# Kernel tuning notes

Measured on AMD Instinct MI355X. Metric: run time of the kernel, lower is better.

## Reference

```python
import jax, jax.numpy as jnp
import numpy as np


def setup_inputs() -> dict:
    key = jax.random.key(0)
    ks = jax.random.split(key, 6)
    B, N, S, D, A = 32, 12, 512, 256, 96
    return {
        "value": jax.random.normal(ks[0], (B, N, S, D), dtype=jnp.float32),
        "emb": jax.random.normal(ks[1], (N, S, A), dtype=jnp.float32),
        "Wqk": jax.random.normal(ks[2], (A, D), dtype=jnp.float32) * (A ** -0.5),
        "bqk": jax.random.normal(ks[3], (D,), dtype=jnp.float32) * 0.02,
        "Wv": jax.random.normal(ks[4], (D, D), dtype=jnp.float32) * (D ** -0.5),
        "bv": jax.random.normal(ks[5], (D,), dtype=jnp.float32) * 0.02,
    }


def reference(value, emb, Wqk, bqk, Wv, bv):
    # qk: [n, s, d] -- query and key share the same projection FC_Q_K
    qk = emb @ Wqk + bqk
    v = value @ Wv + bv                      # [b, n, s, d]
    q = jax.nn.softmax(qk, axis=-1)          # softmax over d (last dim of query)
    k = jax.nn.softmax(qk.swapaxes(-1, -2), axis=-1)  # [n, d, s], softmax over s
    # key @ value: [n, d, s] x [b, n, s, e] -> [b, n, d, e] (broadcast over b)
    kv = jnp.einsum('nds,bnse->bnde', k, v)
    # query @ kv: [n, s, d] x [b, n, d, e] -> [b, n, s, e]
    out = jnp.einsum('nsd,bnde->bnse', q, kv)
    return out
```

## Files before the change

kernel.cpp:

```cpp
#include <hip/hip_runtime.h>
#include <hip/hip_bf16.h>

#define B_ 32
#define N_ 12
#define S_ 512
#define D_ 256
#define A_ 96

typedef __attribute__((ext_vector_type(8))) short short8;
typedef __attribute__((ext_vector_type(4))) float float4v;

static __device__ __forceinline__ ushort f2bf(float f) {
  union { float f; unsigned u; } a;
  a.f = f;
  return (ushort)((a.u + 0x7FFFu + ((a.u >> 16) & 1u)) >> 16);
}

__global__ __launch_bounds__(256) void k_qk_softmax_q(
    const float* __restrict__ emb, const float* __restrict__ Wqk,
    const float* __restrict__ bqk, float* __restrict__ qk,
    ushort* __restrict__ qb) {
  const int blk = blockIdx.x;
  const int tid = threadIdx.x;
  const int d = tid;
  const int wv = tid >> 6, lane = tid & 63;
  __shared__ float seT[A_][8];
  __shared__ float redm[8][4], reds[8][4];
  const float* ebase = emb + (size_t)blk * 8 * A_;
  for (int k = tid; k < 8 * A_; k += 256) {
    int r = k / A_, a = k - r * A_;
    seT[a][r] = ebase[k];
  }
  __syncthreads();
  float bq = bqk[d];
  float acc[8];
#pragma unroll
  for (int r = 0; r < 8; ++r) acc[r] = bq;
#pragma unroll 8
  for (int a = 0; a < A_; ++a) {
    float w = Wqk[a * D_ + d];
    float4 lo = *(const float4*)(&seT[a][0]);
    float4 hi = *(const float4*)(&seT[a][4]);
    acc[0] = fmaf(lo.x, w, acc[0]);
    acc[1] = fmaf(lo.y, w, acc[1]);
    acc[2] = fmaf(lo.z, w, acc[2]);
    acc[3] = fmaf(lo.w, w, acc[3]);
    acc[4] = fmaf(hi.x, w, acc[4]);
    acc[5] = fmaf(hi.y, w, acc[5]);
    acc[6] = fmaf(hi.z, w, acc[6]);
    acc[7] = fmaf(hi.w, w, acc[7]);
  }
  const size_t obase = (size_t)blk * 8 * D_ + d;
#pragma unroll
  for (int r = 0; r < 8; ++r) qk[obase + r * D_] = acc[r];
  float m[8];
#pragma unroll
  for (int r = 0; r < 8; ++r) {
    m[r] = acc[r];
    for (int off = 32; off; off >>= 1) m[r] = fmaxf(m[r], __shfl_xor(m[r], off));
  }
  if (lane == 0) {
#pragma unroll
    for (int r = 0; r < 8; ++r) redm[r][wv] = m[r];
  }
  __syncthreads();
  float e[8], s[8];
#pragma unroll
  for (int r = 0; r < 8; ++r) {
    float mm = fmaxf(fmaxf(redm[r][0], redm[r][1]),
                     fmaxf(redm[r][2], redm[r][3]));
    e[r] = __expf(acc[r] - mm);
    s[r] = e[r];
    for (int off = 32; off; off >>= 1) s[r] += __shfl_xor(s[r], off);
  }
  if (lane == 0) {
#pragma unroll
    for (int r = 0; r < 8; ++r) reds[r][wv] = s[r];
  }
  __syncthreads();
#pragma unroll
  for (int r = 0; r < 8; ++r) {
    float sum = reds[r][0] + reds[r][1] + reds[r][2] + reds[r][3];
    qb[obase + r * D_] = f2bf(e[r] / sum);
  }
}

__global__ __launch_bounds__(256) void k_softmax_kT(
    const float* __restrict__ qk, ushort* __restrict__ kTb) {
  const int dc = blockIdx.x * 16;
  const int n = blockIdx.y;
  const int tid = threadIdx.x;
  __shared__ float t[16][514];
  const float* base = qk + (size_t)n * S_ * D_ + dc;
#pragma unroll
  for (int it = 0; it < 8; ++it) {
    int id = it * 256 + tid;
    int d4 = id & 3, s = id >> 2;
    float4 v = *(const float4*)(base + (size_t)s * D_ + 4 * d4);
    t[4 * d4 + 0][s] = v.x;
    t[4 * d4 + 1][s] = v.y;
    t[4 * d4 + 2][s] = v.z;
    t[4 * d4 + 3][s] = v.w;
  }
  __syncthreads();
  const int d = tid >> 4, sg = tid & 15;
  float vv[32];
  float m = -1e30f;
#pragma unroll
  for (int k = 0; k < 32; ++k) {
    vv[k] = t[d][sg + 16 * k];
    m = fmaxf(m, vv[k]);
  }
  for (int off = 1; off < 16; off <<= 1) m = fmaxf(m, __shfl_xor(m, off));
  float sum = 0.0f;
#pragma unroll
  for (int k = 0; k < 32; ++k) {
    vv[k] = __expf(vv[k] - m);
    sum += vv[k];
  }
  for (int off = 1; off < 16; off <<= 1) sum += __shfl_xor(sum, off);
  float inv = 1.0f / sum;
  const size_t ob = ((size_t)n * D_ + dc + d) * S_;
#pragma unroll
  for (int k = 0; k < 32; ++k) kTb[ob + sg + 16 * k] = f2bf(vv[k] * inv);
}

__global__ __launch_bounds__(256) void k_wvt(const float* __restrict__ Wv,
                                             ushort* __restrict__ WvT) {
  int c = blockIdx.x, e = threadIdx.x;
  WvT[c * D_ + e] = f2bf(Wv[e * D_ + c]);
}

__global__ __launch_bounds__(512) void k_kv0(
    const ushort* __restrict__ kTb, const float* __restrict__ value,
    ushort* __restrict__ kv0) {
  const int f = blockIdx.x;
  const int wk = (f & 7) * 192 + (f >> 3);
  const int eq = wk & 3;
  const int bz = wk >> 2;
  const int n = bz % N_;
  const int tid = threadIdx.x;
  const int l = tid & 63, w = tid >> 6;
  const int lane16 = l & 15, quad = l >> 4;

  __shared__ ushort ldsV[2][64 * 72];

  const int se = tid & 63;
  const int sch = tid >> 6;
  const int schs = (sch ^ ((se >> 3) & 7)) << 3;
  const float* vbase = value + (size_t)bz * S_ * D_ + eq * 64 + se;
  const ushort* kTbase = kTb + (size_t)n * D_ * S_ + (w * 32) * S_;

  float4v acc[4][2];
#pragma unroll
  for (int i = 0; i < 4; ++i)
#pragma unroll
    for (int j = 0; j < 2; ++j) acc[i][j] = (float4v)0.0f;

  union Pack { ushort u[8]; uint4 v; };

  {
    float f0[8];
#pragma unroll
    for (int t = 0; t < 8; ++t) f0[t] = vbase[(size_t)(sch * 8 + t) * D_];
    Pack pk;
#pragma unroll
    for (int t = 0; t < 8; ++t) pk.u[t] = f2bf(f0[t]);
    *(uint4*)(&ldsV[0][se * 72 + schs]) = pk.v;
  }

  int p = 0;
  for (int sc = 0; sc < S_; sc += 64) {
    __syncthreads();
    float fs[8];
    const bool more = (sc + 64 < S_);
    if (more) {
#pragma unroll
      for (int t = 0; t < 8; ++t)
        fs[t] = vbase[(size_t)(sc + 64 + sch * 8 + t) * D_];
    }
#pragma unroll
    for (int kc = 0; kc < 64; kc += 32) {
      const int ko = kc + quad * 8;
      const int chr = ko >> 3;
      short8 a[4], b[2];
#pragma unroll
      for (int i = 0; i < 4; ++i) {
        int er = i * 16 + lane16;
        a[i] = *(const short8*)(
            &ldsV[p][er * 72 + ((chr ^ ((er >> 3) & 7)) << 3)]);
      }
#pragma unroll
      for (int j = 0; j < 2; ++j)
        b[j] = *(const short8*)(kTbase + (j * 16 + lane16) * S_ + sc + ko);
#pragma unroll
      for (int i = 0; i < 4; ++i)
#pragma unroll
        for (int j = 0; j < 2; ++j)
          acc[i][j] = __builtin_amdgcn_mfma_f32_16x16x32_bf16(a[i], b[j],
                                                              acc[i][j], 0, 0, 0);
    }
    if (more) {
      Pack pk;
#pragma unroll
      for (int t = 0; t < 8; ++t) pk.u[t] = f2bf(fs[t]);
      *(uint4*)(&ldsV[p ^ 1][se * 72 + schs]) = pk.v;
    }
    p ^= 1;
  }
  ushort* obase = kv0 + (size_t)bz * D_ * D_;
#pragma unroll
  for (int i = 0; i < 4; ++i) {
#pragma unroll
    for (int j = 0; j < 2; ++j) {
      int d = w * 32 + j * 16 + lane16;
      int e0 = eq * 64 + i * 16 + quad * 4;
      ushort4 pk;
      pk.x = f2bf(acc[i][j][0]);
      pk.y = f2bf(acc[i][j][1]);
      pk.z = f2bf(acc[i][j][2]);
      pk.w = f2bf(acc[i][j][3]);
      *(ushort4*)(obase + d * D_ + e0) = pk;
    }
  }
}

__global__ __launch_bounds__(256) void k_kvw_inplace(
    ushort* kv0, const ushort* __restrict__ WvT,
    const float* __restrict__ bv) {
  const int qd = blockIdx.x;
  const int bz = blockIdx.y;
  const int tid = threadIdx.x;
  const int l = tid & 63, w = tid >> 6;
  const int lane16 = l & 15, quad = l >> 4;

  __shared__ ushort ldsA[64 * 72];
  __shared__ ushort ldsB[256 * 72];

  float4v acc[4][4];
#pragma unroll
  for (int i = 0; i < 4; ++i)
#pragma unroll
    for (int j = 0; j < 4; ++j) acc[i][j] = (float4v)0.0f;

  ushort* base = kv0 + (size_t)bz * (D_ * D_) + qd * (64 * D_);

  for (int ec = 0; ec < D_; ec += 64) {
    __syncthreads();
#pragma unroll
    for (int it = 0; it < 2; ++it) {
      int id = it * 256 + tid;
      int rd = id >> 3, cc = (id & 7) * 8;
      *(uint4*)(&ldsA[rd * 72 + cc]) =
          *(const uint4*)(base + rd * D_ + ec + cc);
    }
#pragma unroll
    for (int it = 0; it < 8; ++it) {
      int id = it * 256 + tid;
      int rd = id >> 3, cc = (id & 7) * 8;
      *(uint4*)(&ldsB[rd * 72 + cc]) =
          *(const uint4*)(WvT + rd * D_ + ec + cc);
    }
    __syncthreads();
#pragma unroll
    for (int kc = 0; kc < 64; kc += 32) {
      int ko = kc + quad * 8;
      short8 a[4], b[4];
#pragma unroll
      for (int i = 0; i < 4; ++i)
        a[i] = *(const short8*)(&ldsA[(i * 16 + lane16) * 72 + ko]);
#pragma unroll
      for (int j = 0; j < 4; ++j)
        b[j] = *(const short8*)(&ldsB[(w * 64 + j * 16 + lane16) * 72 + ko]);
#pragma unroll
      for (int i = 0; i < 4; ++i)
#pragma unroll
        for (int j = 0; j < 4; ++j)
          acc[i][j] = __builtin_amdgcn_mfma_f32_16x16x32_bf16(a[i], b[j],
                                                              acc[i][j], 0, 0, 0);
    }
  }
#pragma unroll
  for (int i = 0; i < 4; ++i) {
#pragma unroll
    for (int j = 0; j < 4; ++j) {
      int c = w * 64 + j * 16 + lane16;
      int d0 = i * 16 + quad * 4;
      float bvc = bv[c];
      ushort4 p;
      p.x = f2bf(acc[i][j][0] + bvc);
      p.y = f2bf(acc[i][j][1] + bvc);
      p.z = f2bf(acc[i][j][2] + bvc);
      p.w = f2bf(acc[i][j][3] + bvc);
      *(ushort4*)(base + c * 64 + d0) = p;
    }
  }
}

__global__ __launch_bounds__(256) void k_out(
    const ushort* __restrict__ qb, const ushort* __restrict__ kvw,
    float* __restrict__ out) {
  const int f = blockIdx.x;
  const int wk = (f & 7) * 384 + (f >> 3);
  const int bx = wk & 3;
  const int by = (wk >> 2) & 1;
  const int bz = wk >> 3;
  const int n = bz % N_;
  const int tid = threadIdx.x;
  const int l = tid & 63, w = tid >> 6;
  const int wm = w & 1, wn = w >> 1;
  const int lane16 = l & 15, quad = l >> 4;

  __shared__ ushort ldsA[128 * 72];
  __shared__ ushort ldsB[128 * 72];

  float4v acc[4][4];
#pragma unroll
  for (int i = 0; i < 4; ++i)
#pragma unroll
    for (int j = 0; j < 4; ++j) acc[i][j] = (float4v)0.0f;

  const ushort* abase = qb + (size_t)n * S_ * D_ + bx * 128 * D_;
  const ushort* bbase = kvw + (size_t)bz * D_ * D_;

  for (int dc = 0; dc < D_; dc += 64) {
    __syncthreads();
#pragma unroll
    for (int it = 0; it < 4; ++it) {
      int id = it * 256 + tid;
      int rd = id >> 3, cc = (id & 7) * 8;
      *(uint4*)(&ldsA[rd * 72 + cc]) =
          *(const uint4*)(abase + rd * D_ + dc + cc);
    }
#pragma unroll
    for (int it = 0; it < 4; ++it) {
      int id = it * 256 + tid;
      int rd = id >> 3, cc = (id & 7) * 8;
      *(uint4*)(&ldsB[rd * 72 + cc]) =
          *(const uint4*)(bbase + (dc >> 6) * 16384 + (by * 128 + rd) * 64 +
                          cc);
    }
    __syncthreads();
#pragma unroll
    for (int kc = 0; kc < 64; kc += 32) {
      int ko = kc + quad * 8;
      short8 a[4], b[4];
#pragma unroll
      for (int i = 0; i < 4; ++i)
        a[i] = *(const short8*)(&ldsA[(wm * 64 + i * 16 + lane16) * 72 + ko]);
#pragma unroll
      for (int j = 0; j < 4; ++j)
        b[j] = *(const short8*)(&ldsB[(wn * 64 + j * 16 + lane16) * 72 + ko]);
#pragma unroll
      for (int i = 0; i < 4; ++i)
#pragma unroll
        for (int j = 0; j < 4; ++j)
          acc[i][j] = __builtin_amdgcn_mfma_f32_16x16x32_bf16(a[i], b[j],
                                                              acc[i][j], 0, 0, 0);
    }
  }
  float* obase = out + (size_t)bz * S_ * D_;
#pragma unroll
  for (int i = 0; i < 4; ++i) {
#pragma unroll
    for (int j = 0; j < 4; ++j) {
      int s0 = bx * 128 + wm * 64 + i * 16 + quad * 4;
      int c = by * 128 + wn * 64 + j * 16 + lane16;
#pragma unroll
      for (int r = 0; r < 4; ++r)
        obase[(s0 + r) * D_ + c] = acc[i][j][r];
    }
  }
}

extern "C" void kernel_launch(void* const* d_in, const int* in_sizes, int n_in,
                              void* d_out, int out_size, void* d_ws,
                              size_t ws_size, hipStream_t stream) {
  const float* value = (const float*)d_in[0];
  const float* emb   = (const float*)d_in[1];
  const float* Wqk   = (const float*)d_in[2];
  const float* bqk   = (const float*)d_in[3];
  const float* Wv    = (const float*)d_in[4];
  const float* bv    = (const float*)d_in[5];
  float* out = (float*)d_out;

  char* ws = (char*)d_ws;
  float*  qk  = (float*)ws;
  ushort* qb  = (ushort*)(ws + 6291456);
  ushort* kTb = (ushort*)(ws + 9437184);
  ushort* kv0 = (ushort*)(ws + 12582912);
  ushort* WvT = (ushort*)(ws + 62914560);

  k_qk_softmax_q<<<dim3(N_ * S_ / 8), 256, 0, stream>>>(emb, Wqk, bqk, qk, qb);
  k_softmax_kT<<<dim3(16, N_), 256, 0, stream>>>(qk, kTb);
  k_wvt<<<dim3(D_), 256, 0, stream>>>(Wv, WvT);
  k_kv0<<<dim3(4 * B_ * N_), 512, 0, stream>>>(kTb, value, kv0);
  k_kvw_inplace<<<dim3(4, B_ * N_), 256, 0, stream>>>(kv0, WvT, bv);
  k_out<<<dim3(4 * 2 * B_ * N_), 256, 0, stream>>>(qb, kv0, out);
}
```

Before: 449.8 us.

## Use direct global-to-LDS loads with XOR swizzle in GEMM kernels; shrink softmax tiles

In k_kvw_inplace and k_out, the register-staged global-to-LDS copies become global_load_lds 16-byte direct loads. The LDS tiles change from padded 72-element rows to unpadded 64-element rows, with an XOR chunk swizzle that avoids bank conflicts. Separately, k_softmax_kT now handles 4 columns per block instead of 16, launching four times as many blocks to raise parallelism. The direct loads bypass VGPRs and cut instruction count, but the per-wave row addressing and swizzle must match the LDS layout exactly.

```diff
diff --git a/kernel.cpp b/kernel.cpp
--- a/kernel.cpp
+++ b/kernel.cpp
@@ -14,6 +14,12 @@
   union { float f; unsigned u; } a;
   a.f = f;
   return (ushort)((a.u + 0x7FFFu + ((a.u >> 16) & 1u)) >> 16);
+}
+
+static __device__ __forceinline__ void gload16(const ushort* g, ushort* l) {
+  __builtin_amdgcn_global_load_lds(
+      (const __attribute__((address_space(1))) unsigned int*)g,
+      (__attribute__((address_space(3))) unsigned int*)l, 16, 0, 0);
 }
 
 __global__ __launch_bounds__(256) void k_qk_softmax_q(
@@ -87,42 +93,41 @@
 
 __global__ __launch_bounds__(256) void k_softmax_kT(
     const float* __restrict__ qk, ushort* __restrict__ kTb) {
-  const int dc = blockIdx.x * 16;
+  const int dc = blockIdx.x * 4;
   const int n = blockIdx.y;
   const int tid = threadIdx.x;
-  __shared__ float t[16][514];
+  __shared__ float t[4][514];
   const float* base = qk + (size_t)n * S_ * D_ + dc;
 #pragma unroll
-  for (int it = 0; it < 8; ++it) {
-    int id = it * 256 + tid;
-    int d4 = id & 3, s = id >> 2;
-    float4 v = *(const float4*)(base + (size_t)s * D_ + 4 * d4);
-    t[4 * d4 + 0][s] = v.x;
-    t[4 * d4 + 1][s] = v.y;
-    t[4 * d4 + 2][s] = v.z;
-    t[4 * d4 + 3][s] = v.w;
+  for (int it = 0; it < 2; ++it) {
+    int s = it * 256 + tid;
+    float4 v = *(const float4*)(base + (size_t)s * D_);
+    t[0][s] = v.x;
+    t[1][s] = v.y;
+    t[2][s] = v.z;
+    t[3][s] = v.w;
   }
   __syncthreads();
-  const int d = tid >> 4, sg = tid & 15;
-  float vv[32];
+  const int d = tid >> 6, sg = tid & 63;
+  float vv[8];
   float m = -1e30f;
 #pragma unroll
-  for (int k = 0; k < 32; ++k) {
-    vv[k] = t[d][sg + 16 * k];
+  for (int k = 0; k < 8; ++k) {
+    vv[k] = t[d][sg + 64 * k];
     m = fmaxf(m, vv[k]);
   }
-  for (int off = 1; off < 16; off <<= 1) m = fmaxf(m, __shfl_xor(m, off));
+  for (int off = 32; off; off >>= 1) m = fmaxf(m, __shfl_xor(m, off));
   float sum = 0.0f;
 #pragma unroll
-  for (int k = 0; k < 32; ++k) {
+  for (int k = 0; k < 8; ++k) {
     vv[k] = __expf(vv[k] - m);
     sum += vv[k];
   }
-  for (int off = 1; off < 16; off <<= 1) sum += __shfl_xor(sum, off);
+  for (int off = 32; off; off >>= 1) sum += __shfl_xor(sum, off);
   float inv = 1.0f / sum;
   const size_t ob = ((size_t)n * D_ + dc + d) * S_;
 #pragma unroll
-  for (int k = 0; k < 32; ++k) kTb[ob + sg + 16 * k] = f2bf(vv[k] * inv);
+  for (int k = 0; k < 8; ++k) kTb[ob + sg + 64 * k] = f2bf(vv[k] * inv);
 }
 
 __global__ __launch_bounds__(256) void k_wvt(const float* __restrict__ Wv,
@@ -233,9 +238,10 @@
   const int tid = threadIdx.x;
   const int l = tid & 63, w = tid >> 6;
   const int lane16 = l & 15, quad = l >> 4;
-
-  __shared__ ushort ldsA[64 * 72];
-  __shared__ ushort ldsB[256 * 72];
+  const int srow = l >> 3, chp = l & 7;
+
+  __shared__ ushort ldsA[64 * 64];
+  __shared__ ushort ldsB[256 * 64];
 
   float4v acc[4][4];
 #pragma unroll
@@ -248,30 +254,33 @@
   for (int ec = 0; ec < D_; ec += 64) {
     __syncthreads();
 #pragma unroll
-    for (int it = 0; it < 2; ++it) {
-      int id = it * 256 + tid;
-      int rd = id >> 3, cc = (id & 7) * 8;
-      *(uint4*)(&ldsA[rd * 72 + cc]) =
-          *(const uint4*)(base + rd * D_ + ec + cc);
-    }
-#pragma unroll
-    for (int it = 0; it < 8; ++it) {
-      int id = it * 256 + tid;
-      int rd = id >> 3, cc = (id & 7) * 8;
-      *(uint4*)(&ldsB[rd * 72 + cc]) =
-          *(const uint4*)(WvT + rd * D_ + ec + cc);
+    for (int i = 0; i < 2; ++i) {
+      int r = w * 16 + i * 8 + srow;
+      gload16(base + (size_t)r * D_ + ec + ((chp ^ (r & 7)) << 3),
+              &ldsA[(w * 16 + i * 8) * 64]);
+    }
+#pragma unroll
+    for (int i = 0; i < 8; ++i) {
+      int r = w * 64 + i * 8 + srow;
+      gload16(WvT + (size_t)r * D_ + ec + ((chp ^ (r & 7)) << 3),
+              &ldsB[(w * 64 + i * 8) * 64]);
     }
     __syncthreads();
 #pragma unroll
     for (int kc = 0; kc < 64; kc += 32) {
       int ko = kc + quad * 8;
+      int chr = ko >> 3;
       short8 a[4], b[4];
 #pragma unroll
-      for (int i = 0; i < 4; ++i)
-        a[i] = *(const short8*)(&ldsA[(i * 16 + lane16) * 72 + ko]);
-#pragma unroll
-      for (int j = 0; j < 4; ++j)
-        b[j] = *(const short8*)(&ldsB[(w * 64 + j * 16 + lane16) * 72 + ko]);
+      for (int i = 0; i < 4; ++i) {
+        int rr = i * 16 + lane16;
+        a[i] = *(const short8*)(&ldsA[rr * 64 + ((chr ^ (rr & 7)) << 3)]);
+      }
+#pragma unroll
+      for (int j = 0; j < 4; ++j) {
+        int rc = w * 64 + j * 16 + lane16;
+        b[j] = *(const short8*)(&ldsB[rc * 64 + ((chr ^ (rc & 7)) << 3)]);
+      }
 #pragma unroll
       for (int i = 0; i < 4; ++i)
 #pragma unroll
@@ -310,9 +319,10 @@
   const int l = tid & 63, w = tid >> 6;
   const int wm = w & 1, wn = w >> 1;
   const int lane16 = l & 15, quad = l >> 4;
-
-  __shared__ ushort ldsA[128 * 72];
-  __shared__ ushort ldsB[128 * 72];
+  const int srow = l >> 3, chp = l & 7;
+
+  __shared__ ushort ldsA[128 * 64];
+  __shared__ ushort ldsB[128 * 64];
 
   float4v acc[4][4];
 #pragma unroll
@@ -326,31 +336,34 @@
   for (int dc = 0; dc < D_; dc += 64) {
     __syncthreads();
 #pragma unroll
-    for (int it = 0; it < 4; ++it) {
-      int id = it * 256 + tid;
-      int rd = id >> 3, cc = (id & 7) * 8;
-      *(uint4*)(&ldsA[rd * 72 + cc]) =
-          *(const uint4*)(abase + rd * D_ + dc + cc);
-    }
-#pragma unroll
-    for (int it = 0; it < 4; ++it) {
-      int id = it * 256 + tid;
-      int rd = id >> 3, cc = (id & 7) * 8;
-      *(uint4*)(&ldsB[rd * 72 + cc]) =
-          *(const uint4*)(bbase + (dc >> 6) * 16384 + (by * 128 + rd) * 64 +
-                          cc);
+    for (int i = 0; i < 4; ++i) {
+      int r = w * 32 + i * 8 + srow;
+      gload16(abase + (size_t)r * D_ + dc + ((chp ^ (r & 7)) << 3),
+              &ldsA[(w * 32 + i * 8) * 64]);
+    }
+#pragma unroll
+    for (int i = 0; i < 4; ++i) {
+      int r = w * 32 + i * 8 + srow;
+      gload16(bbase + (dc >> 6) * 16384 + (by * 128 + r) * 64 +
+                  ((chp ^ (r & 7)) << 3),
+              &ldsB[(w * 32 + i * 8) * 64]);
     }
     __syncthreads();
 #pragma unroll
     for (int kc = 0; kc < 64; kc += 32) {
       int ko = kc + quad * 8;
+      int chr = ko >> 3;
       short8 a[4], b[4];
 #pragma unroll
-      for (int i = 0; i < 4; ++i)
-        a[i] = *(const short8*)(&ldsA[(wm * 64 + i * 16 + lane16) * 72 + ko]);
-#pragma unroll
-      for (int j = 0; j < 4; ++j)
-        b[j] = *(const short8*)(&ldsB[(wn * 64 + j * 16 + lane16) * 72 + ko]);
+      for (int i = 0; i < 4; ++i) {
+        int rr = wm * 64 + i * 16 + lane16;
+        a[i] = *(const short8*)(&ldsA[rr * 64 + ((chr ^ (rr & 7)) << 3)]);
+      }
+#pragma unroll
+      for (int j = 0; j < 4; ++j) {
+        int rc = wn * 64 + j * 16 + lane16;
+        b[j] = *(const short8*)(&ldsB[rc * 64 + ((chr ^ (rc & 7)) << 3)]);
+      }
 #pragma unroll
       for (int i = 0; i < 4; ++i)
 #pragma unroll
@@ -392,7 +405,7 @@
   ushort* WvT = (ushort*)(ws + 62914560);
 
   k_qk_softmax_q<<<dim3(N_ * S_ / 8), 256, 0, stream>>>(emb, Wqk, bqk, qk, qb);
-  k_softmax_kT<<<dim3(16, N_), 256, 0, stream>>>(qk, kTb);
+  k_softmax_kT<<<dim3(64, N_), 256, 0, stream>>>(qk, kTb);
   k_wvt<<<dim3(D_), 256, 0, stream>>>(Wv, WvT);
   k_kv0<<<dim3(4 * B_ * N_), 512, 0, stream>>>(kTb, value, kv0);
   k_kvw_inplace<<<dim3(4, B_ * N_), 256, 0, stream>>>(kv0, WvT, bv);
```

Result: no change. 458.5 us (+1.9%).
